# Optimization experiments

Measured on AMD Instinct MI355X. Metric: run time of the kernel, lower is better.

The kernel has to match this reference:

```python
import jax, jax.numpy as jnp
import numpy as np

IMG = 512
STRIDE = 16
K = 9
FM = IMG // STRIDE          # 32
N = FM * FM * K             # 9216 anchors
IOU_THR = 0.7
POST_NMS_TOPK = 300
C_FEAT = 512


def _conv(x, w, b, stride=1, padding='SAME'):
    y = jax.lax.conv_general_dilated(x, w, (stride, stride), padding,
                                     dimension_numbers=('NCHW', 'OIHW', 'NCHW'))
    return y + b[None, :, None, None]


def _make_anchors():
    scales = [64.0, 128.0, 256.0]
    ratios = [0.5, 1.0, 2.0]
    wh = np.array([[s * np.sqrt(r), s / np.sqrt(r)] for s in scales for r in ratios],
                  np.float32)                                    # [K,2]
    ctr = (np.arange(FM, dtype=np.float32) + 0.5) * STRIDE
    cy, cx = np.meshgrid(ctr, ctr, indexing='ij')               # [FM,FM]
    c = np.stack([cx, cy], -1)[:, :, None, :]                   # [FM,FM,1,2]
    half = wh[None, None, :, :] / 2.0                           # [1,1,K,2]
    boxes = np.concatenate([c - half, c + half], -1)            # [FM,FM,K,4]
    return boxes.reshape(-1, 4)


def setup_inputs():
    key = jax.random.key(0)
    ks = jax.random.split(key, 5)
    p = lambda k, shp, s: jax.random.normal(k, shp, jnp.float32) * s
    return {
        'input_image': jax.random.normal(ks[0], (1, 3, IMG, IMG), jnp.float32),
        'anchors': jnp.asarray(_make_anchors()),
        'w_bb': p(ks[1], (C_FEAT, 3, STRIDE, STRIDE), 0.05),
        'b_bb': jnp.zeros((C_FEAT,), jnp.float32),
        'w_rpn': p(ks[2], (C_FEAT, C_FEAT, 3, 3), 0.02),
        'b_rpn': jnp.zeros((C_FEAT,), jnp.float32),
        'w_cls': p(ks[3], (2 * K, C_FEAT, 1, 1), 0.01),
        'b_cls': jnp.zeros((2 * K,), jnp.float32),
        'w_box': p(ks[4], (4 * K, C_FEAT, 1, 1), 0.01),
        'b_box': jnp.zeros((4 * K,), jnp.float32),
    }


def _decode_clip(anchors, deltas):
    # apply_delta_to_anchors + clip_boxes
    wa = anchors[:, 2] - anchors[:, 0]
    ha = anchors[:, 3] - anchors[:, 1]
    cxa = anchors[:, 0] + 0.5 * wa
    cya = anchors[:, 1] + 0.5 * ha
    dx, dy = deltas[:, 0], deltas[:, 1]
    dw = jnp.clip(deltas[:, 2], -4.0, 4.0)   # numeric guard on exp
    dh = jnp.clip(deltas[:, 3], -4.0, 4.0)
    cx = cxa + dx * wa
    cy = cya + dy * ha
    w = wa * jnp.exp(dw)
    h = ha * jnp.exp(dh)
    x1 = jnp.maximum(cx - 0.5 * w, 0.0)
    y1 = jnp.maximum(cy - 0.5 * h, 0.0)
    x2 = jnp.minimum(cx + 0.5 * w, IMG - 1.0)
    y2 = jnp.minimum(cy + 0.5 * h, IMG - 1.0)
    return jnp.stack([x1, y1, x2, y2], -1)


def _iou_matrix(b):
    x1, y1, x2, y2 = b[:, 0], b[:, 1], b[:, 2], b[:, 3]
    area = (x2 - x1) * (y2 - y1)
    iw = jnp.clip(jnp.minimum(x2[:, None], x2[None, :]) - jnp.maximum(x1[:, None], x1[None, :]), 0.0)
    ih = jnp.clip(jnp.minimum(y2[:, None], y2[None, :]) - jnp.maximum(y1[:, None], y1[None, :]), 0.0)
    inter = iw * ih
    return inter / (area[:, None] + area[None, :] - inter + 1e-9)


def _nms_keep(boxes_sorted):
    # boxes_sorted: [N,4] in descending score order; greedy hard NMS.
    iou = jax.lax.stop_gradient(_iou_matrix(boxes_sorted))  # [N,N]
    idx = jnp.arange(N)

    def body(i, keep):
        sup = keep[i] & (iou[i] > IOU_THR) & (idx > i)
        return keep & ~sup

    return jax.lax.fori_loop(0, N, body, jnp.ones((N,), bool))


def reference(input_image, anchors, w_bb, b_bb, w_rpn, b_rpn, w_cls, b_cls, w_box, b_box):
    # backbone
    feat = jax.nn.relu(_conv(input_image, w_bb, b_bb, stride=STRIDE, padding='VALID'))  # [1,512,32,32]
    # rpn
    hid = jax.nn.relu(_conv(feat, w_rpn, b_rpn))
    cls = _conv(hid, w_cls, b_cls)   # [1,2K,FM,FM]
    box = _conv(hid, w_box, b_box)   # [1,4K,FM,FM]
    # foreground scores: cls_scores[:, k:, :, :]
    scores = cls[0, K:, :, :].transpose(1, 2, 0).reshape(-1)                    # [N]
    deltas = box[0].reshape(K, 4, FM, FM).transpose(2, 3, 0, 1).reshape(-1, 4)  # [N,4]
    proposals = _decode_clip(anchors, deltas)
    order = jnp.argsort(-scores)
    boxes_s = proposals[order]
    keep = _nms_keep(boxes_s)
    # first 300 kept boxes (score order); fixed shape via stable argsort on keep flag
    sel = jnp.argsort((~keep).astype(jnp.int32), stable=True)[:POST_NMS_TOPK]
    return boxes_s[sel]
```

## Files before the change

kernel.cpp:

```cpp
#include <hip/hip_runtime.h>
#include <stdint.h>

typedef unsigned long long u64;

#define PTOT 1024
#define CF   512
#define NBOX 9216
#define NPAD 9280
#define NW   144
#define TOPK 300
#define RCH  19

__device__ __forceinline__ uint32_t score_key(float s) {
  uint32_t b = __float_as_uint(s);
  uint32_t o = (b & 0x80000000u) ? ~b : (b | 0x80000000u);
  return ~o;
}

#define FMA16() do { \
  acc[0][0] = fmaf(bv.x, av.x, acc[0][0]); \
  acc[0][1] = fmaf(bv.x, av.y, acc[0][1]); \
  acc[0][2] = fmaf(bv.x, av.z, acc[0][2]); \
  acc[0][3] = fmaf(bv.x, av.w, acc[0][3]); \
  acc[1][0] = fmaf(bv.y, av.x, acc[1][0]); \
  acc[1][1] = fmaf(bv.y, av.y, acc[1][1]); \
  acc[1][2] = fmaf(bv.y, av.z, acc[1][2]); \
  acc[1][3] = fmaf(bv.y, av.w, acc[1][3]); \
  acc[2][0] = fmaf(bv.z, av.x, acc[2][0]); \
  acc[2][1] = fmaf(bv.z, av.y, acc[2][1]); \
  acc[2][2] = fmaf(bv.z, av.z, acc[2][2]); \
  acc[2][3] = fmaf(bv.z, av.w, acc[2][3]); \
  acc[3][0] = fmaf(bv.w, av.x, acc[3][0]); \
  acc[3][1] = fmaf(bv.w, av.y, acc[3][1]); \
  acc[3][2] = fmaf(bv.w, av.z, acc[3][2]); \
  acc[3][3] = fmaf(bv.w, av.w, acc[3][3]); \
} while (0)

__global__ __launch_bounds__(256) void k_front(const float* __restrict__ w_rpn,
                                               const float* __restrict__ w_bb,
                                               const float* __restrict__ img,
                                               float* __restrict__ wT,
                                               float* __restrict__ featP) {
  __shared__ __align__(16) float As[32][72];
  __shared__ __align__(16) float Bs[32][64];
  __shared__ float Twt[32][33];
  const int bid = blockIdx.x;
  const int t = threadIdx.x;

  if (bid < 2304) {
    const int kb = (bid >> 4) * 32;
    const int cob = (bid & 15) * 32;
    const int tx = t & 31, ty = t >> 5;
#pragma unroll
    for (int r = 0; r < 32; r += 8)
      Twt[ty + r][tx] = w_rpn[(cob + ty + r) * 4608 + kb + tx];
    __syncthreads();
#pragma unroll
    for (int r = 0; r < 32; r += 8)
      wT[(kb + ty + r) * 512 + cob + tx] = Twt[tx][ty + r];
    return;
  }

  const int b2 = bid - 2304;
  const int pbase = (b2 & 15) * 64;
  const int cobase = ((b2 >> 4) & 7) * 64;
  const int z = b2 >> 7;
  const int pg = t & 15, cg = t >> 4;
  const int pp0 = pg * 4, cc0 = cg * 4;
  const int py0 = pbase >> 5;
  float acc[4][4] = {};
  for (int kb = 0; kb < 256; kb += 32) {
    const int ky0 = kb >> 4;
#pragma unroll
    for (int l0 = 0; l0 < 2048; l0 += 256) {
      int l = l0 + t;
      int seg = l >> 9, off = l & 511;
      int py_off = seg >> 1, ky_off = seg & 1;
      int row = (py0 + py_off) * 16 + ky0 + ky_off;
      float v = img[(z * 512 + row) * 512 + off];
      As[ky_off * 16 + (off & 15)][py_off * 32 + (off >> 4)] = v;
    }
#pragma unroll
    for (int it = 0; it < 2; ++it) {
      int idx4 = it * 256 + t;
      int co = idx4 & 63;
      int k4 = (idx4 >> 6) * 4;
      float4 v = *(const float4*)&w_bb[(size_t)(cobase + co) * 768 + z * 256 + kb + k4];
      Bs[k4 + 0][co] = v.x;
      Bs[k4 + 1][co] = v.y;
      Bs[k4 + 2][co] = v.z;
      Bs[k4 + 3][co] = v.w;
    }
    __syncthreads();
#pragma unroll
    for (int kk = 0; kk < 32; ++kk) {
      float4 av = *(const float4*)&As[kk][pp0];
      float4 bv = *(const float4*)&Bs[kk][cc0];
      FMA16();
    }
    __syncthreads();
  }
#pragma unroll
  for (int i = 0; i < 4; ++i) {
    float* o = &featP[((size_t)z * CF + cobase + cc0 + i) * PTOT + pbase + pp0];
    *(float4*)o = make_float4(acc[i][0], acc[i][1], acc[i][2], acc[i][3]);
  }
}

__global__ __launch_bounds__(128) void k_conv2(const float* __restrict__ featP,
                                               const float* __restrict__ bias1,
                                               const float* __restrict__ wT,
                                               float* __restrict__ hidP,
                                               int ciPerZ) {
  __shared__ __align__(16) float As[8][10][44];
  __shared__ __align__(16) float Bs[72 * 64];
  const int t = threadIdx.x;
  const int pyb = blockIdx.x * 8;
  const int cob = blockIdx.y * 64;
  const int z = blockIdx.z;
  const int cib = z * ciPerZ;
  const int pg = t & 15, cg = t >> 4;
  const int prow = pg >> 1, px0 = (pg & 1) * 16;
  const int co0 = cg * 8;
  float acc[8][16] = {};
  for (int cc = 0; cc < ciPerZ; cc += 8) {
    {
      int idx4 = t;
#pragma unroll
      for (int it = 0; it < 7; ++it, idx4 += 128) {
        if (idx4 < 800) {
          int ci = idx4 / 100;
          int rem = idx4 - ci * 100;
          int row = rem / 10;
          int col4 = (rem - row * 10) << 2;
          int x = col4 - 4;
          int gy = pyb + row - 1;
          float4 v = make_float4(0.f, 0.f, 0.f, 0.f);
          if (x >= 0 && x < 32 && gy >= 0 && gy < 32) {
            const int c = cib + cc + ci;
            const float* f0 = &featP[(size_t)c * PTOT + gy * 32 + x];
            float4 a0 = *(const float4*)f0;
            float4 a1 = *(const float4*)(f0 + (size_t)CF * PTOT);
            float4 a2 = *(const float4*)(f0 + (size_t)2 * CF * PTOT);
            float b = bias1[c];
            v.x = fmaxf(a0.x + a1.x + a2.x + b, 0.f);
            v.y = fmaxf(a0.y + a1.y + a2.y + b, 0.f);
            v.z = fmaxf(a0.z + a1.z + a2.z + b, 0.f);
            v.w = fmaxf(a0.w + a1.w + a2.w + b, 0.f);
          }
          *(float4*)&As[ci][row][col4] = v;
        }
      }
    }
    {
      const int kg0 = (cib + cc) * 9;
      int idx4 = t;
#pragma unroll
      for (int it = 0; it < 9; ++it, idx4 += 128) {
        int k = idx4 >> 4;
        int co4 = (idx4 & 15) << 2;
        *(float4*)&Bs[k * 64 + co4] =
            *(const float4*)&wT[(kg0 + k) * 512 + cob + co4];
      }
    }
    __syncthreads();
#pragma unroll 1
    for (int ci = 0; ci < 8; ++ci) {
#pragma unroll
      for (int dy = 0; dy < 3; ++dy) {
        const float* Ar = &As[ci][prow + dy][px0];
        float rw[24];
        *(float4*)&rw[0]  = *(const float4*)&Ar[0];
        *(float4*)&rw[4]  = *(const float4*)&Ar[4];
        *(float4*)&rw[8]  = *(const float4*)&Ar[8];
        *(float4*)&rw[12] = *(const float4*)&Ar[12];
        *(float4*)&rw[16] = *(const float4*)&Ar[16];
        *(float4*)&rw[20] = *(const float4*)&Ar[20];
#pragma unroll
        for (int dx = 0; dx < 3; ++dx) {
          const float* Bp = &Bs[(ci * 9 + dy * 3 + dx) * 64 + co0];
          float4 b0 = *(const float4*)&Bp[0];
          float4 b1 = *(const float4*)&Bp[4];
          float bm[8] = {b0.x, b0.y, b0.z, b0.w, b1.x, b1.y, b1.z, b1.w};
#pragma unroll
          for (int m = 0; m < 8; ++m)
#pragma unroll
            for (int j = 0; j < 16; ++j)
              acc[m][j] = fmaf(rw[3 + dx + j], bm[m], acc[m][j]);
        }
      }
    }
    __syncthreads();
  }
  const int prowg = pyb + prow;
#pragma unroll
  for (int m = 0; m < 8; ++m) {
    int co = cob + co0 + m;
    float* o = &hidP[((size_t)z * CF + co) * PTOT + prowg * 32 + px0];
    *(float4*)&o[0]  = make_float4(acc[m][0],  acc[m][1],  acc[m][2],  acc[m][3]);
    *(float4*)&o[4]  = make_float4(acc[m][4],  acc[m][5],  acc[m][6],  acc[m][7]);
    *(float4*)&o[8]  = make_float4(acc[m][8],  acc[m][9],  acc[m][10], acc[m][11]);
    *(float4*)&o[12] = make_float4(acc[m][12], acc[m][13], acc[m][14], acc[m][15]);
  }
}

__global__ __launch_bounds__(256) void k_reduce2(const float* __restrict__ hidP,
                                                 const float* __restrict__ bias,
                                                 float* __restrict__ hid_t, int Z) {
  __shared__ float T[32][33];
  const int co0 = blockIdx.x * 32, p0 = blockIdx.y * 32;
  const int t = threadIdx.x;
  {
    int co = t >> 3, p4 = (t & 7) << 2;
    float4 s = make_float4(0.f, 0.f, 0.f, 0.f);
    for (int zz = 0; zz < Z; ++zz) {
      float4 v = *(const float4*)&hidP[((size_t)zz * CF + co0 + co) * PTOT + p0 + p4];
      s.x += v.x; s.y += v.y; s.z += v.z; s.w += v.w;
    }
    float b = bias[co0 + co];
    T[co][p4 + 0] = fmaxf(s.x + b, 0.f);
    T[co][p4 + 1] = fmaxf(s.y + b, 0.f);
    T[co][p4 + 2] = fmaxf(s.z + b, 0.f);
    T[co][p4 + 3] = fmaxf(s.w + b, 0.f);
  }
  __syncthreads();
  {
    int p = t >> 3, co4 = (t & 7) << 2;
    float4 o = make_float4(T[co4][p], T[co4 + 1][p], T[co4 + 2][p], T[co4 + 3][p]);
    *(float4*)&hid_t[(size_t)(p0 + p) * CF + co0 + co4] = o;
  }
}

__global__ __launch_bounds__(256) void k_heads(const float* __restrict__ hid_t,
                                               const float* __restrict__ wcls,
                                               const float* __restrict__ bcls,
                                               const float* __restrict__ wbox,
                                               const float* __restrict__ bbox,
                                               uint32_t* __restrict__ key32,
                                               float* __restrict__ deltas) {
  const int t = threadIdx.x;
  if (blockIdx.x == 256) {
    if (t < 64) key32[NBOX + t] = 0xFFFFFFFFu;
    return;
  }
  const int lane = t & 63, w = t >> 6;
  const int p = blockIdx.x * 4 + w;
  const float* hp = &hid_t[(size_t)p * CF + lane * 8];
  float4 h0 = *(const float4*)hp;
  float4 h1 = *(const float4*)(hp + 4);
#pragma unroll 1
  for (int ch = 0; ch < 45; ++ch) {
    const float* wp = (ch < 9) ? &wcls[(9 + ch) * CF] : &wbox[(ch - 9) * CF];
    float4 w0 = *(const float4*)(wp + lane * 8);
    float4 w1 = *(const float4*)(wp + lane * 8 + 4);
    float s = h0.x * w0.x + h0.y * w0.y + h0.z * w0.z + h0.w * w0.w +
              h1.x * w1.x + h1.y * w1.y + h1.z * w1.z + h1.w * w1.w;
#pragma unroll
    for (int off = 32; off >= 1; off >>= 1) s += __shfl_xor(s, off, 64);
    if (lane == 0) {
      if (ch < 9) key32[p * 9 + ch] = score_key(s + bcls[9 + ch]);
      else        deltas[p * 36 + (ch - 9)] = s + bbox[ch - 9];
    }
  }
}

__global__ __launch_bounds__(256) void k_rank(const uint32_t* __restrict__ key32,
                                              uint32_t* __restrict__ P) {
  const int t = threadIdx.x;
  const int lane = t & 63, w = t >> 6;
  const int a = blockIdx.x * 4 + w;
  if (a >= 145) return;
  const int by = blockIdx.y;
  const int ig = a * 64 + lane;
  const uint32_t ka = key32[ig];
  uint32_t cnt = 0;
#pragma unroll 1
  for (int w2 = 0; w2 < 8; ++w2) {
    int word = by * 8 + w2;
    if (word >= 145) break;
    const uint32_t* bk = &key32[word * 64];
    const int jbase = word * 64;
#pragma unroll
    for (int s = 0; s < 64; ++s) {
      uint32_t kb = bk[s];
      int j = jbase + s;
      cnt += (uint32_t)((kb < ka) || (kb == ka && j < ig));
    }
  }
  P[(size_t)by * NPAD + ig] = cnt;
}

__global__ __launch_bounds__(256) void k_rfin(const uint32_t* __restrict__ P,
                                              const float* __restrict__ anchors,
                                              const float* __restrict__ deltas,
                                              float4* __restrict__ boxesS) {
  int i = blockIdx.x * 256 + threadIdx.x;
  if (i >= NBOX) return;
  uint32_t rank = 0;
#pragma unroll
  for (int c = 0; c < RCH; ++c) rank += P[(size_t)c * NPAD + i];
  float4 a = ((const float4*)anchors)[i];
  float4 d = ((const float4*)deltas)[i];
  float wa = a.z - a.x, ha = a.w - a.y;
  float cxa = a.x + 0.5f * wa, cya = a.y + 0.5f * ha;
  float dw = fminf(fmaxf(d.z, -4.f), 4.f);
  float dh = fminf(fmaxf(d.w, -4.f), 4.f);
  float cx = cxa + d.x * wa, cy = cya + d.y * ha;
  float ww = wa * expf(dw), hh = ha * expf(dh);
  float x1 = fmaxf(cx - 0.5f * ww, 0.f);
  float y1 = fmaxf(cy - 0.5f * hh, 0.f);
  float x2 = fminf(cx + 0.5f * ww, 511.f);
  float y2 = fminf(cy + 0.5f * hh, 511.f);
  boxesS[rank] = make_float4(x1, y1, x2, y2);
}

__global__ __launch_bounds__(256) void k_iou(const float4* __restrict__ boxesS,
                                             u64* __restrict__ mask) {
  __shared__ float4 cb[4][64];
  __shared__ float ca[4][64];
  const int t = threadIdx.x;
  const int lane = t & 63, w = t >> 6;
  const int u = blockIdx.x;
  const int v = blockIdx.y * 4 + w + 1;
  int y = u + v; if (y >= 145) y -= 145;
  const int a_ = min(u, y), b_ = max(u, y);
  const int iw = a_, wj = b_ - 1;

  {
    float4 c = boxesS[wj * 64 + lane];
    cb[w][lane] = c;
    ca[w][lane] = (c.z - c.x) * (c.w - c.y);
  }
  __syncthreads();

  const int i = iw * 64 + lane;
  float4 a = boxesS[i];
  float areaA = (a.z - a.x) * (a.w - a.y);
  u64 bits = 0;
#pragma unroll 4
  for (int jj = 0; jj < 64; ++jj) {
    int j = wj * 64 + jj;
    float4 c = cb[w][jj];
    float iw_ = fmaxf(fminf(a.z, c.z) - fmaxf(a.x, c.x), 0.f);
    float ih_ = fmaxf(fminf(a.w, c.w) - fmaxf(a.y, c.y), 0.f);
    float inter = iw_ * ih_;
    float uni = areaA + ca[w][jj] - inter + 1e-9f;
    float thr = 0.7f * uni;
    bool pos = uni > 0.f;
    bool sup = pos && (inter > thr);
    if (pos && (fabsf(inter - thr) <= thr * 1e-5f))
      sup = (inter / uni) > 0.7f;
    bits |= ((u64)(sup && (j > i))) << jj;
  }
  mask[(size_t)i * NW + wj] = bits;
}

__global__ __launch_bounds__(64) void k_scan(const u64* __restrict__ mask,
                                             const float4* __restrict__ boxesS,
                                             float* __restrict__ out) {
  __shared__ u64 keepArr[NW];
  __shared__ int pf[NW + 2];
  __shared__ int outIdx[TOPK];
  const int lane = threadIdx.x;

  u64 r0 = 0, r1 = 0, r2 = 0;
  int keptCount = 0;
  int stopSpan = NW - 1;

  u64 dcur = mask[(size_t)lane * NW];

  for (int wb = 0; wb < NW; ++wb) {
    u64 v = (wb < 64) ? r0 : ((wb < 128) ? r1 : r2);
    u64 R = __shfl(v, wb & 63, 64);

    u64 dnext = 0;
    if (wb + 1 < NW)
      dnext = mask[(size_t)((wb + 1) * 64 + lane) * NW + (wb + 1)];

    u64 keepmask = 0;
    u64 notR = ~R;
    while (notR) {
      int rl = __ffsll((long long)notR) - 1;
      keepmask |= 1ull << rl;
      u64 drl = __shfl(dcur, rl, 64);
      R |= drl;
      u64 above = (rl >= 63) ? 0ull : (~0ull << (rl + 1));
      notR = ~R & above;
    }

    if (keepmask) {
      u64 km = keepmask;
      while (km) {
        int first = wb * 64 + __ffsll((long long)km) - 1;
        int idx[8];
#pragma unroll
        for (int s = 0; s < 8; ++s) {
          if (km) { idx[s] = wb * 64 + __ffsll((long long)km) - 1; km &= km - 1; }
          else    { idx[s] = first; }
        }
        u64 A[8], B[8], C[8];
#pragma unroll
        for (int s = 0; s < 8; ++s) {
          const u64* q = mask + (size_t)idx[s] * NW;
          A[s] = q[lane];
          B[s] = q[lane + 64];
          C[s] = (lane < 16) ? q[lane + 128] : 0ull;
        }
#pragma unroll
        for (int s = 0; s < 8; ++s) { r0 |= A[s]; r1 |= B[s]; r2 |= C[s]; }
      }
      keptCount += __popcll(keepmask);
    }
    if (lane == 0) keepArr[wb] = keepmask;
    dcur = dnext;
    if (keptCount >= TOPK) { stopSpan = wb; break; }
  }

  __syncthreads();
  if (lane == 0) {
    int acc = 0;
    for (int s = 0; s <= stopSpan; ++s) { pf[s] = acc; acc += __popcll(keepArr[s]); }
    pf[stopSpan + 1] = acc;
  }
  __syncthreads();
  const int keptTotal = pf[stopSpan + 1];

  for (int s = lane; s <= stopSpan; s += 64) {
    u64 km = keepArr[s];
    int slot = pf[s];
    while (km && slot < TOPK) {
      int rl = __ffsll((long long)km) - 1; km &= km - 1;
      outIdx[slot++] = s * 64 + rl;
    }
  }
  if (keptTotal < TOPK) {
    for (int s = lane; s <= stopSpan; s += 64) {
      u64 rm = ~keepArr[s];
      int slot = keptTotal + s * 64 - pf[s];
      while (rm && slot < TOPK) {
        int rl = __ffsll((long long)rm) - 1; rm &= rm - 1;
        outIdx[slot++] = s * 64 + rl;
      }
    }
  }
  __syncthreads();
#pragma unroll
  for (int k0 = 0; k0 < TOPK + 63; k0 += 64) {
    int k = k0 + lane;
    if (k < TOPK) {
      float4 bx = boxesS[outIdx[k]];
      out[k * 4 + 0] = bx.x;
      out[k * 4 + 1] = bx.y;
      out[k * 4 + 2] = bx.z;
      out[k * 4 + 3] = bx.w;
    }
  }
}

extern "C" void kernel_launch(void* const* d_in, const int* in_sizes, int n_in,
                              void* d_out, int out_size, void* d_ws, size_t ws_size,
                              hipStream_t stream) {
  const float* img   = (const float*)d_in[0];
  const float* anch  = (const float*)d_in[1];
  const float* w_bb  = (const float*)d_in[2];
  const float* b_bb  = (const float*)d_in[3];
  const float* w_rpn = (const float*)d_in[4];
  const float* b_rpn = (const float*)d_in[5];
  const float* w_cls = (const float*)d_in[6];
  const float* b_cls = (const float*)d_in[7];
  const float* w_box = (const float*)d_in[8];
  const float* b_box = (const float*)d_in[9];

  char* ws = (char*)d_ws;
  int Z = 16;
  if (ws_size < 22806528ull + 16ull * 2097152ull) Z = 8;
  if (ws_size < 22806528ull + 8ull * 2097152ull)  Z = 4;
  if (ws_size < 22806528ull + 4ull * 2097152ull)  Z = 2;
  if (ws_size < 22806528ull + 2ull * 2097152ull)  Z = 1;

  float* wT    = (float*)(ws);
  float* featP = (float*)(ws + 9437184);
  float* hidP  = (float*)(ws + 15728640);
  char*  hte   = ws + 15728640 + (size_t)Z * 2097152;
  float* hid_t = (float*)hte;
  char*  tail  = hte + 2097152;
  float*    deltas = (float*)(tail);
  uint32_t* key32  = (uint32_t*)(tail + 0x28000);
  float4*   boxesS = (float4*)(tail + 0x38000);
  uint32_t* P      = (uint32_t*)(ws + 9437184);
  u64*      mask   = (u64*)(ws);
  float*    out    = (float*)d_out;

  hipLaunchKernelGGL(k_front, dim3(2688), dim3(256), 0, stream, w_rpn, w_bb, img, wT, featP);
  hipLaunchKernelGGL(k_conv2, dim3(4, 8, Z), dim3(128), 0, stream, featP, b_bb, wT, hidP, 512 / Z);
  hipLaunchKernelGGL(k_reduce2, dim3(16, 32), dim3(256), 0, stream, hidP, b_rpn, hid_t, Z);
  hipLaunchKernelGGL(k_heads, dim3(257), dim3(256), 0, stream, hid_t, w_cls, b_cls, w_box, b_box, key32, deltas);
  hipLaunchKernelGGL(k_rank, dim3(37, RCH), dim3(256), 0, stream, key32, P);
  hipLaunchKernelGGL(k_rfin, dim3(37), dim3(256), 0, stream, P, anch, deltas, boxesS);
  hipLaunchKernelGGL(k_iou, dim3(145, 18), dim3(256), 0, stream, boxesS, mask);
  hipLaunchKernelGGL(k_scan, dim3(1), dim3(64), 0, stream, mask, boxesS, out);
}
```

Baseline: 327.2 us.

## Split conv2 input channels across two half-blocks with shared-memory reduction

Doubles the conv2 block size to 256 threads, with each 128-thread half handling half of the block's input-channel range in its own shared-memory A/B tiles. The upper half writes its partial accumulators to shared memory and the lower half adds them before storing to the partial output buffer. The aim is more waves in flight per tile, which helps latency hiding on a small grid. The cost is roughly double the shared-memory footprint, an extra sync, and a shared-memory reduction step.

```diff
diff --git a/kernel.cpp b/kernel.cpp
--- a/kernel.cpp
+++ b/kernel.cpp
@@ -107,25 +107,29 @@
   }
 }
 
-__global__ __launch_bounds__(128) void k_conv2(const float* __restrict__ featP,
+__global__ __launch_bounds__(256) void k_conv2(const float* __restrict__ featP,
                                                const float* __restrict__ bias1,
                                                const float* __restrict__ wT,
                                                float* __restrict__ hidP,
                                                int ciPerZ) {
-  __shared__ __align__(16) float As[8][10][44];
-  __shared__ __align__(16) float Bs[72 * 64];
+  __shared__ __align__(16) float SH[16512];
   const int t = threadIdx.x;
+  const int h = t >> 7;
+  const int tl = t & 127;
   const int pyb = blockIdx.x * 8;
   const int cob = blockIdx.y * 64;
   const int z = blockIdx.z;
-  const int cib = z * ciPerZ;
-  const int pg = t & 15, cg = t >> 4;
+  const int halfCi = ciPerZ >> 1;
+  const int cib = z * ciPerZ + h * halfCi;
+  const int pg = tl & 15, cg = tl >> 4;
   const int prow = pg >> 1, px0 = (pg & 1) * 16;
   const int co0 = cg * 8;
+  float* Abase = SH + h * 3520;
+  float* Bbase = SH + 7040 + h * 4608;
   float acc[8][16] = {};
-  for (int cc = 0; cc < ciPerZ; cc += 8) {
+  for (int cc = 0; cc < halfCi; cc += 8) {
     {
-      int idx4 = t;
+      int idx4 = tl;
 #pragma unroll
       for (int it = 0; it < 7; ++it, idx4 += 128) {
         if (idx4 < 800) {
@@ -148,18 +152,18 @@
             v.z = fmaxf(a0.z + a1.z + a2.z + b, 0.f);
             v.w = fmaxf(a0.w + a1.w + a2.w + b, 0.f);
           }
-          *(float4*)&As[ci][row][col4] = v;
+          *(float4*)&Abase[ci * 440 + row * 44 + col4] = v;
         }
       }
     }
     {
       const int kg0 = (cib + cc) * 9;
-      int idx4 = t;
+      int idx4 = tl;
 #pragma unroll
       for (int it = 0; it < 9; ++it, idx4 += 128) {
         int k = idx4 >> 4;
         int co4 = (idx4 & 15) << 2;
-        *(float4*)&Bs[k * 64 + co4] =
+        *(float4*)&Bbase[k * 64 + co4] =
             *(const float4*)&wT[(kg0 + k) * 512 + cob + co4];
       }
     }
@@ -168,7 +172,7 @@
     for (int ci = 0; ci < 8; ++ci) {
 #pragma unroll
       for (int dy = 0; dy < 3; ++dy) {
-        const float* Ar = &As[ci][prow + dy][px0];
+        const float* Ar = &Abase[ci * 440 + (prow + dy) * 44 + px0];
         float rw[24];
         *(float4*)&rw[0]  = *(const float4*)&Ar[0];
         *(float4*)&rw[4]  = *(const float4*)&Ar[4];
@@ -178,7 +182,7 @@
         *(float4*)&rw[20] = *(const float4*)&Ar[20];
 #pragma unroll
         for (int dx = 0; dx < 3; ++dx) {
-          const float* Bp = &Bs[(ci * 9 + dy * 3 + dx) * 64 + co0];
+          const float* Bp = &Bbase[(ci * 9 + dy * 3 + dx) * 64 + co0];
           float4 b0 = *(const float4*)&Bp[0];
           float4 b1 = *(const float4*)&Bp[4];
           float bm[8] = {b0.x, b0.y, b0.z, b0.w, b1.x, b1.y, b1.z, b1.w};
@@ -192,15 +196,29 @@
     }
     __syncthreads();
   }
-  const int prowg = pyb + prow;
-#pragma unroll
-  for (int m = 0; m < 8; ++m) {
-    int co = cob + co0 + m;
-    float* o = &hidP[((size_t)z * CF + co) * PTOT + prowg * 32 + px0];
-    *(float4*)&o[0]  = make_float4(acc[m][0],  acc[m][1],  acc[m][2],  acc[m][3]);
-    *(float4*)&o[4]  = make_float4(acc[m][4],  acc[m][5],  acc[m][6],  acc[m][7]);
-    *(float4*)&o[8]  = make_float4(acc[m][8],  acc[m][9],  acc[m][10], acc[m][11]);
-    *(float4*)&o[12] = make_float4(acc[m][12], acc[m][13], acc[m][14], acc[m][15]);
+  float4* SH4 = (float4*)SH;
+  if (h == 1) {
+#pragma unroll
+    for (int m = 0; m < 8; ++m)
+#pragma unroll
+      for (int q = 0; q < 4; ++q)
+        SH4[(m * 4 + q) * 128 + tl] =
+            make_float4(acc[m][q*4], acc[m][q*4+1], acc[m][q*4+2], acc[m][q*4+3]);
+  }
+  __syncthreads();
+  if (h == 0) {
+    const int prowg = pyb + prow;
+#pragma unroll
+    for (int m = 0; m < 8; ++m) {
+      int co = cob + co0 + m;
+      float* o = &hidP[((size_t)z * CF + co) * PTOT + prowg * 32 + px0];
+#pragma unroll
+      for (int q = 0; q < 4; ++q) {
+        float4 p = SH4[(m * 4 + q) * 128 + tl];
+        *(float4*)&o[q * 4] = make_float4(acc[m][q*4] + p.x, acc[m][q*4+1] + p.y,
+                                          acc[m][q*4+2] + p.z, acc[m][q*4+3] + p.w);
+      }
+    }
   }
 }
 
@@ -492,7 +510,7 @@
   float*    out    = (float*)d_out;
 
   hipLaunchKernelGGL(k_front, dim3(2688), dim3(256), 0, stream, w_rpn, w_bb, img, wT, featP);
-  hipLaunchKernelGGL(k_conv2, dim3(4, 8, Z), dim3(128), 0, stream, featP, b_bb, wT, hidP, 512 / Z);
+  hipLaunchKernelGGL(k_conv2, dim3(4, 8, Z), dim3(256), 0, stream, featP, b_bb, wT, hidP, 512 / Z);
   hipLaunchKernelGGL(k_reduce2, dim3(16, 32), dim3(256), 0, stream, hidP, b_rpn, hid_t, Z);
   hipLaunchKernelGGL(k_heads, dim3(257), dim3(256), 0, stream, hid_t, w_cls, b_cls, w_box, b_box, key32, deltas);
   hipLaunchKernelGGL(k_rank, dim3(37, RCH), dim3(256), 0, stream, key32, P);
```

Result: no change. 331.8 us (+1.4%).
